# Optimization experiments

Hardware: AMD Instinct MI355X
Metric: run time of the kernel (lower is better)

Reference implementation:

```python
import jax, jax.numpy as jnp
import numpy as np

N = 100000
E = 3200000
IN_DIM = 64
HID = 64
G = 4096
BN_EPS = 1e-5


def setup_inputs() -> dict:
    key = jax.random.key(0)
    ks = jax.random.split(key, 20)
    def lin(k, fi, fo):
        bound = 1.0 / np.sqrt(fi)
        kw, kb = jax.random.split(k)
        W = jax.random.uniform(kw, (fi, fo), jnp.float32, -bound, bound)
        b = jax.random.uniform(kb, (fo,), jnp.float32, -bound, bound)
        return W, b
    x = jax.random.normal(ks[0], (N, IN_DIM), jnp.float32)
    edge_index = jax.random.randint(ks[1], (2, E), 0, N, jnp.int64)
    batch = jnp.sort(jax.random.randint(ks[2], (N,), 0, G, jnp.int64))
    proj_W, proj_b = lin(ks[3], IN_DIM, HID)
    conv1_W, conv1_b = lin(ks[4], HID, HID)
    conv2_W, conv2_b = lin(ks[5], HID, HID)
    conv3_W, conv3_b = lin(ks[6], HID, HID)
    head_W1, head_b1 = lin(ks[7], HID, HID // 2)
    head_W2, head_b2 = lin(ks[8], HID // 2, 1)
    ones = jnp.ones((HID,), jnp.float32)
    zeros = jnp.zeros((HID,), jnp.float32)
    return dict(
        x=x, edge_index=edge_index, batch=batch,
        proj_W=proj_W, proj_b=proj_b,
        conv1_W=conv1_W, conv1_b=conv1_b,
        conv2_W=conv2_W, conv2_b=conv2_b,
        conv3_W=conv3_W, conv3_b=conv3_b,
        bn1_g=ones, bn1_b=zeros, bn2_g=ones, bn2_b=zeros,
        bn3_g=ones, bn3_b=zeros,
        head_W1=head_W1, head_b1=head_b1,
        head_W2=head_W2, head_b2=head_b2,
    )


def _gcn_conv(x, W, b, src, dst, dinv):
    # GCNConv with self-loops and symmetric normalization (PyG semantics).
    xl = x @ W                                   # [N, H]
    norm = dinv[src] * dinv[dst]                 # [E]
    msg = xl[src] * norm[:, None]                # [E, H]  (memory-bound gather)
    agg = jax.ops.segment_sum(msg, dst, num_segments=x.shape[0])
    agg = agg + (dinv * dinv)[:, None] * xl      # self-loop contribution
    return agg + b


def _bn(h, g, b):
    mu = jnp.mean(h, axis=0)
    var = jnp.var(h, axis=0)
    return (h - mu) * jax.lax.rsqrt(var + BN_EPS) * g + b


def reference(x, edge_index, batch,
              proj_W, proj_b,
              conv1_W, conv1_b, conv2_W, conv2_b, conv3_W, conv3_b,
              bn1_g, bn1_b, bn2_g, bn2_b, bn3_g, bn3_b,
              head_W1, head_b1, head_W2, head_b2):
    src, dst = edge_index[0], edge_index[1]
    n = x.shape[0]
    # degree including self loop
    deg = jax.ops.segment_sum(jnp.ones_like(dst, jnp.float32), dst, num_segments=n) + 1.0
    dinv = jax.lax.rsqrt(deg)

    x0 = jax.nn.relu(x @ proj_W + proj_b)
    h = jax.nn.relu(_bn(_gcn_conv(x0, conv1_W, conv1_b, src, dst, dinv), bn1_g, bn1_b))
    h = jax.nn.relu(_bn(_gcn_conv(h, conv2_W, conv2_b, src, dst, dinv), bn2_g, bn2_b))
    h = h + x0
    h = jax.nn.relu(_bn(_gcn_conv(h, conv3_W, conv3_b, src, dst, dinv), bn3_g, bn3_b))

    # global mean pool over graphs
    sums = jax.ops.segment_sum(h, batch, num_segments=G)
    cnts = jax.ops.segment_sum(jnp.ones((n,), jnp.float32), batch, num_segments=G)
    pooled = sums / jnp.maximum(cnts, 1.0)[:, None]

    out = jax.nn.relu(pooled @ head_W1 + head_b1) @ head_W2 + head_b2
    return out.squeeze(-1)
```

## Files before the change

kernel.cpp:

```cpp
#include <hip/hip_runtime.h>
#include <hip/hip_fp16.h>

#define NNODES 100000
#define NEDGES 3200000
#define NGRAPH 4096
#define SBCNT 196
#define SBCAP 17504
#define P1CHUNK 4096
#define P1CAP 56
#define P1GRID 782
#define AGG_GRID 2048
#define BN_EPS 1e-5f
#define INV_N (1.0f / 100000.0f)

__global__ void k_zero_i(int* __restrict__ p, int n) {
  int i = blockIdx.x * blockDim.x + threadIdx.x;
  int st = gridDim.x * blockDim.x;
  for (; i < n; i += st) p[i] = 0;
}
__global__ void k_zero_f(float* __restrict__ p, int n) {
  int i = blockIdx.x * blockDim.x + threadIdx.x;
  int st = gridDim.x * blockDim.x;
  for (; i < n; i += st) p[i] = 0.0f;
}

__global__ void k_part1(const int* __restrict__ src, const int* __restrict__ dst,
                        int* __restrict__ sbcur, int* __restrict__ sbbuf, int e) {
  __shared__ int cnt[SBCNT];
  __shared__ int base[SBCNT];
  __shared__ int bins[SBCNT * P1CAP];
  int t = threadIdx.x;
  int start = blockIdx.x * P1CHUNK;
  int end = min(start + P1CHUNK, e);
  for (int i = t; i < SBCNT; i += 256) cnt[i] = 0;
  __syncthreads();
  for (int i = start + t; i < end; i += 256) {
    int s = src[i], d = dst[i];
    int sb = d >> 9;
    int en = (s << 9) | (d & 511);
    int pos = atomicAdd(&cnt[sb], 1);
    if (pos < P1CAP) {
      bins[sb * P1CAP + pos] = en;
    } else {
      int gp = atomicAdd(&sbcur[sb], 1);
      if (gp < SBCAP) sbbuf[(size_t)sb * SBCAP + gp] = en;
    }
  }
  __syncthreads();
  if (t < SBCNT) {
    int c = min(cnt[t], P1CAP);
    base[t] = (c > 0) ? atomicAdd(&sbcur[t], c) : 0;
  }
  __syncthreads();
  int lane = t & 63, wid = t >> 6;
  for (int b = wid; b < SBCNT; b += 4) {
    int c = min(cnt[b], P1CAP);
    if (lane < c) {
      int gp = base[b] + lane;
      if (gp < SBCAP) sbbuf[(size_t)b * SBCAP + gp] = bins[b * P1CAP + lane];
    }
  }
}

__global__ void k_part2(const int* __restrict__ sbcur, const int* __restrict__ sbbuf,
                        int* __restrict__ slots, int* __restrict__ deg,
                        int* __restrict__ rowstart, float* __restrict__ dinv) {
  __shared__ int cnt[512];
  __shared__ int pfx[512];
  __shared__ int cur[512];
  int sb = blockIdx.x;
  int t = threadIdx.x;
  int n = min(sbcur[sb], SBCAP);
  const int* __restrict__ pb = sbbuf + (size_t)sb * SBCAP;
  cnt[t] = 0;
  __syncthreads();
  for (int i = t; i < n; i += 512) atomicAdd(&cnt[pb[i] & 511], 1);
  __syncthreads();
  int myc = cnt[t];
  pfx[t] = myc;
  __syncthreads();
  for (int o = 1; o < 512; o <<= 1) {
    int x = (t >= o) ? pfx[t - o] : 0;
    __syncthreads();
    pfx[t] += x;
    __syncthreads();
  }
  int excl = pfx[t] - myc;
  int node = sb * 512 + t;
  if (node < NNODES) {
    deg[node] = myc;
    rowstart[node] = sb * SBCAP + excl;
    dinv[node] = rsqrtf((float)myc + 1.0f);
  }
  cur[t] = 0;
  __syncthreads();
  pfx[t] = excl;
  __syncthreads();
  for (int i = t; i < n; i += 512) {
    int e = pb[i];
    int dl = e & 511;
    int pos = atomicAdd(&cur[dl], 1);
    slots[(size_t)sb * SBCAP + pfx[dl] + pos] = e >> 9;
  }
}

template <int PRO, bool A_HALF, bool EPI_DINV, bool EPI_BR>
__global__ void k_gemm64(const void* __restrict__ Ain, const float* __restrict__ W,
                         const float* __restrict__ bias, const float* __restrict__ stats,
                         const float* __restrict__ g, const float* __restrict__ bb,
                         const __half* __restrict__ res, const float* __restrict__ dinv,
                         __half* __restrict__ C, int n) {
  __shared__ float Ws[64 * 64];
  __shared__ float As[64 * 64];
  __shared__ float scs[64], shs[64], bs[64];
  int t = threadIdx.x;
  {
    const float4* W4 = (const float4*)W;
    float4* Ws4 = (float4*)Ws;
    for (int i = t; i < 1024; i += 256) Ws4[i] = W4[i];
  }
  if (t < 64) {
    if (EPI_BR) bs[t] = bias[t];
    if (PRO >= 1) {
      float mu = stats[t] * INV_N;
      float var = stats[64 + t] * INV_N - mu * mu;
      float sc = g[t] * rsqrtf(var + BN_EPS);
      scs[t] = sc;
      shs[t] = bb[t] - mu * sc;
    }
  }
  int row0 = blockIdx.x * 64;
  int rows = min(64, n - row0);
  __syncthreads();
  if constexpr (A_HALF) {
    const __half2* A2 = (const __half2*)((const __half*)Ain + (size_t)row0 * 64);
    const __half2* R2 = (PRO == 2) ? (const __half2*)(res + (size_t)row0 * 64) : nullptr;
    for (int i = t; i < rows * 32; i += 256) {
      float2 f = __half22float2(A2[i]);
      int r = i >> 5;
      int c0 = (i & 31) * 2;
      if (PRO >= 1) {
        f.x = fmaxf(fmaf(f.x, scs[c0], shs[c0]), 0.0f);
        f.y = fmaxf(fmaf(f.y, scs[c0 + 1], shs[c0 + 1]), 0.0f);
        if (PRO == 2) {
          float2 r2 = __half22float2(R2[i]);
          f.x += r2.x;
          f.y += r2.y;
        }
      }
      As[r * 64 + c0] = f.x;
      As[r * 64 + c0 + 1] = f.y;
    }
  } else {
    const float4* A4 = (const float4*)((const float*)Ain + (size_t)row0 * 64);
    float4* As4 = (float4*)As;
    for (int i = t; i < rows * 16; i += 256) As4[i] = A4[i];
  }
  __syncthreads();
  int c = t & 63;
  int w = t >> 6;
  float acc[16];
#pragma unroll
  for (int j = 0; j < 16; ++j) acc[j] = 0.0f;
#pragma unroll 4
  for (int k = 0; k < 64; ++k) {
    float wv = Ws[(k << 6) + c];
#pragma unroll
    for (int j = 0; j < 16; ++j) {
      acc[j] = fmaf(As[((w + 4 * j) << 6) + k], wv, acc[j]);
    }
  }
#pragma unroll
  for (int j = 0; j < 16; ++j) {
    int r = w + 4 * j;
    if (r < rows) {
      float o = acc[j];
      if (EPI_BR) o = fmaxf(o + bs[c], 0.0f);
      if (EPI_DINV) o *= dinv[row0 + r];
      C[(size_t)(row0 + r) * 64 + c] = __float2half(o);
    }
  }
}

__global__ __launch_bounds__(256, 8)
void k_agg(const int* __restrict__ deg, const int* __restrict__ rowstart,
           const int* __restrict__ slots, const __half* __restrict__ y,
           const float* __restrict__ dinv, __half* __restrict__ ag,
           float* __restrict__ pstats) {
  int t = threadIdx.x;
  int lane = t & 63, wid = t >> 6;
  int wave = blockIdx.x * 4 + wid;
  int nw = gridDim.x * 4;
  float s = 0.0f, q = 0.0f;
  for (int node0 = wave; node0 < NNODES; node0 += nw) {
    int node = __builtin_amdgcn_readfirstlane(node0);
    int m = deg[node];
    const int* __restrict__ sp = slots + rowstart[node];
    float a0 = __half2float(y[(size_t)node * 64 + lane]);
    float a1 = 0.0f, a2 = 0.0f, a3 = 0.0f;
    float a4 = 0.0f, a5 = 0.0f, a6 = 0.0f, a7 = 0.0f;
    int k = 0;
    for (; k + 24 <= m; k += 24) {
      int i00 = sp[k + 0],  i01 = sp[k + 1],  i02 = sp[k + 2],  i03 = sp[k + 3];
      int i04 = sp[k + 4],  i05 = sp[k + 5],  i06 = sp[k + 6],  i07 = sp[k + 7];
      int i08 = sp[k + 8],  i09 = sp[k + 9],  i10 = sp[k + 10], i11 = sp[k + 11];
      int i12 = sp[k + 12], i13 = sp[k + 13], i14 = sp[k + 14], i15 = sp[k + 15];
      int i16 = sp[k + 16], i17 = sp[k + 17], i18 = sp[k + 18], i19 = sp[k + 19];
      int i20 = sp[k + 20], i21 = sp[k + 21], i22 = sp[k + 22], i23 = sp[k + 23];
      __half v00 = y[(size_t)i00 * 64 + lane];
      __half v01 = y[(size_t)i01 * 64 + lane];
      __half v02 = y[(size_t)i02 * 64 + lane];
      __half v03 = y[(size_t)i03 * 64 + lane];
      __half v04 = y[(size_t)i04 * 64 + lane];
      __half v05 = y[(size_t)i05 * 64 + lane];
      __half v06 = y[(size_t)i06 * 64 + lane];
      __half v07 = y[(size_t)i07 * 64 + lane];
      __half v08 = y[(size_t)i08 * 64 + lane];
      __half v09 = y[(size_t)i09 * 64 + lane];
      __half v10 = y[(size_t)i10 * 64 + lane];
      __half v11 = y[(size_t)i11 * 64 + lane];
      __half v12 = y[(size_t)i12 * 64 + lane];
      __half v13 = y[(size_t)i13 * 64 + lane];
      __half v14 = y[(size_t)i14 * 64 + lane];
      __half v15 = y[(size_t)i15 * 64 + lane];
      __half v16 = y[(size_t)i16 * 64 + lane];
      __half v17 = y[(size_t)i17 * 64 + lane];
      __half v18 = y[(size_t)i18 * 64 + lane];
      __half v19 = y[(size_t)i19 * 64 + lane];
      __half v20 = y[(size_t)i20 * 64 + lane];
      __half v21 = y[(size_t)i21 * 64 + lane];
      __half v22 = y[(size_t)i22 * 64 + lane];
      __half v23 = y[(size_t)i23 * 64 + lane];
      a0 += __half2float(v00); a1 += __half2float(v01);
      a2 += __half2float(v02); a3 += __half2float(v03);
      a4 += __half2float(v04); a5 += __half2float(v05);
      a6 += __half2float(v06); a7 += __half2float(v07);
      a0 += __half2float(v08); a1 += __half2float(v09);
      a2 += __half2float(v10); a3 += __half2float(v11);
      a4 += __half2float(v12); a5 += __half2float(v13);
      a6 += __half2float(v14); a7 += __half2float(v15);
      a0 += __half2float(v16); a1 += __half2float(v17);
      a2 += __half2float(v18); a3 += __half2float(v19);
      a4 += __half2float(v20); a5 += __half2float(v21);
      a6 += __half2float(v22); a7 += __half2float(v23);
    }
    for (; k + 8 <= m; k += 8) {
      int i0 = sp[k + 0], i1 = sp[k + 1], i2 = sp[k + 2], i3 = sp[k + 3];
      int i4 = sp[k + 4], i5 = sp[k + 5], i6 = sp[k + 6], i7 = sp[k + 7];
      __half v0 = y[(size_t)i0 * 64 + lane];
      __half v1 = y[(size_t)i1 * 64 + lane];
      __half v2 = y[(size_t)i2 * 64 + lane];
      __half v3 = y[(size_t)i3 * 64 + lane];
      __half v4 = y[(size_t)i4 * 64 + lane];
      __half v5 = y[(size_t)i5 * 64 + lane];
      __half v6 = y[(size_t)i6 * 64 + lane];
      __half v7 = y[(size_t)i7 * 64 + lane];
      a0 += __half2float(v0); a1 += __half2float(v1);
      a2 += __half2float(v2); a3 += __half2float(v3);
      a4 += __half2float(v4); a5 += __half2float(v5);
      a6 += __half2float(v6); a7 += __half2float(v7);
    }
    for (; k + 4 <= m; k += 4) {
      int i0 = sp[k + 0], i1 = sp[k + 1], i2 = sp[k + 2], i3 = sp[k + 3];
      __half v0 = y[(size_t)i0 * 64 + lane];
      __half v1 = y[(size_t)i1 * 64 + lane];
      __half v2 = y[(size_t)i2 * 64 + lane];
      __half v3 = y[(size_t)i3 * 64 + lane];
      a0 += __half2float(v0); a1 += __half2float(v1);
      a2 += __half2float(v2); a3 += __half2float(v3);
    }
    for (; k < m; ++k) a0 += __half2float(y[(size_t)sp[k] * 64 + lane]);
    float o = dinv[node] * (((a0 + a1) + (a2 + a3)) + ((a4 + a5) + (a6 + a7)));
    ag[(size_t)node0 * 64 + lane] = __float2half(o);
    s += o;
    q = fmaf(o, o, q);
  }
  __shared__ float ls[256], lq[256];
  ls[t] = s;
  lq[t] = q;
  __syncthreads();
  if (t < 64) {
    pstats[blockIdx.x * 128 + t] = ls[t] + ls[64 + t] + ls[128 + t] + ls[192 + t];
    pstats[blockIdx.x * 128 + 64 + t] = lq[t] + lq[64 + t] + lq[128 + t] + lq[192 + t];
  }
}

__global__ void k_stats_reduce(const float* __restrict__ pstats, float* __restrict__ stats) {
  __shared__ float red[256];
  int c = blockIdx.x;
  int t = threadIdx.x;
  float s = 0.0f;
  for (int i = t; i < AGG_GRID; i += 256) s += pstats[i * 128 + c];
  red[t] = s;
  __syncthreads();
  for (int o = 128; o >= 1; o >>= 1) {
    if (t < o) red[t] += red[t + o];
    __syncthreads();
  }
  if (t == 0) stats[c] = red[0];
}

__global__ void k_pool(const __half* __restrict__ ag, const float* __restrict__ stats,
                       const float* __restrict__ g, const float* __restrict__ bb,
                       const int* __restrict__ batch, float* __restrict__ psum,
                       float* __restrict__ pcnt) {
  int t = threadIdx.x, lane = t & 63;
  int wave = blockIdx.x * 4 + (t >> 6);
  int c0 = wave * 32;
  if (c0 >= NNODES) return;
  float mu = stats[lane] * INV_N;
  float var = stats[64 + lane] * INV_N - mu * mu;
  float sc = g[lane] * rsqrtf(var + BN_EPS);
  float sh = bb[lane] - mu * sc;
  int gprev = -1;
  float av = 0.0f, cv = 0.0f;
  int end = min(c0 + 32, NNODES);
  for (int node = c0; node < end; ++node) {
    int gi = batch[node];
    if (gi != gprev) {
      if (gprev >= 0) {
        atomicAdd(&psum[gprev * 64 + lane], av);
        if (lane == 0) atomicAdd(&pcnt[gprev], cv);
      }
      gprev = gi;
      av = 0.0f;
      cv = 0.0f;
    }
    av += fmaxf(fmaf(__half2float(ag[(size_t)node * 64 + lane]), sc, sh), 0.0f);
    cv += 1.0f;
  }
  if (gprev >= 0) {
    atomicAdd(&psum[gprev * 64 + lane], av);
    if (lane == 0) atomicAdd(&pcnt[gprev], cv);
  }
}

__global__ void k_head(const float* __restrict__ psum, const float* __restrict__ pcnt,
                       const float* __restrict__ W1, const float* __restrict__ b1,
                       const float* __restrict__ W2, const float* __restrict__ b2,
                       float* __restrict__ out) {
  int gidx = blockIdx.x;
  int t = threadIdx.x;
  __shared__ float pooled[64];
  __shared__ float hid[32];
  float cnt = fmaxf(pcnt[gidx], 1.0f);
  pooled[t] = psum[gidx * 64 + t] / cnt;
  __syncthreads();
  if (t < 32) {
    float a = b1[t];
#pragma unroll
    for (int k = 0; k < 64; ++k) a = fmaf(pooled[k], W1[k * 32 + t], a);
    hid[t] = fmaxf(a, 0.0f);
  }
  __syncthreads();
  if (t == 0) {
    float o = b2[0];
#pragma unroll
    for (int j = 0; j < 32; ++j) o = fmaf(hid[j], W2[j], o);
    out[gidx] = o;
  }
}

extern "C" void kernel_launch(void* const* d_in, const int* in_sizes, int n_in,
                              void* d_out, int out_size, void* d_ws, size_t ws_size,
                              hipStream_t stream) {
  const float* x       = (const float*)d_in[0];
  const int*   eidx    = (const int*)d_in[1];
  const int*   batch   = (const int*)d_in[2];
  const float* proj_W  = (const float*)d_in[3];
  const float* proj_b  = (const float*)d_in[4];
  const float* conv1_W = (const float*)d_in[5];
  const float* conv2_W = (const float*)d_in[7];
  const float* conv3_W = (const float*)d_in[9];
  const float* bn1_g   = (const float*)d_in[11];
  const float* bn1_b   = (const float*)d_in[12];
  const float* bn2_g   = (const float*)d_in[13];
  const float* bn2_b   = (const float*)d_in[14];
  const float* bn3_g   = (const float*)d_in[15];
  const float* bn3_b   = (const float*)d_in[16];
  const float* head_W1 = (const float*)d_in[17];
  const float* head_b1 = (const float*)d_in[18];
  const float* head_W2 = (const float*)d_in[19];
  const float* head_b2 = (const float*)d_in[20];
  float* out = (float*)d_out;

  const int N = NNODES, E = NEDGES, G = NGRAPH;
  const int* src = eidx;
  const int* dst = eidx + E;

  char* p = (char*)d_ws;
  auto align256 = [](size_t v) { return (v + 255) & ~(size_t)255; };
  int* sbcur = (int*)p;       p += align256((size_t)SBCNT * 4);
  int* deg = (int*)p;         p += align256((size_t)N * 4);
  int* rowstart = (int*)p;    p += align256((size_t)N * 4);
  int* slots = (int*)p;       p += align256((size_t)SBCNT * SBCAP * 4);
  float* dinv = (float*)p;    p += align256((size_t)N * 4);
  __half* x016 = (__half*)p;  p += align256((size_t)N * 64 * 2);
  __half* y16 = (__half*)p;   p += align256((size_t)N * 64 * 2);
  __half* ag16 = (__half*)p;  p += align256((size_t)N * 64 * 2);
  float* pstats = (float*)p;  p += align256((size_t)AGG_GRID * 128 * 4);
  float* stats1 = (float*)p;  p += align256(128 * 4);
  float* stats2 = (float*)p;  p += align256(128 * 4);
  float* stats3 = (float*)p;  p += align256(128 * 4);
  float* psum = (float*)p;    p += align256((size_t)G * 64 * 4);
  float* pcnt = (float*)p;    p += align256((size_t)G * 4);
  int* sbbuf = (int*)y16;

  const int TB = 256;
  int gemm_grid = (N + 63) / 64;

  k_zero_i<<<1, SBCNT, 0, stream>>>(sbcur, SBCNT);
  k_part1<<<P1GRID, TB, 0, stream>>>(src, dst, sbcur, sbbuf, E);
  k_part2<<<SBCNT, 512, 0, stream>>>(sbcur, sbbuf, slots, deg, rowstart, dinv);

  k_zero_f<<<(G * 64 + G + TB - 1) / TB, TB, 0, stream>>>(psum, G * 64 + G);

  k_gemm64<0, false, false, true><<<gemm_grid, TB, 0, stream>>>(
      x, proj_W, proj_b, nullptr, nullptr, nullptr, nullptr, nullptr, x016, N);

  k_gemm64<0, true, true, false><<<gemm_grid, TB, 0, stream>>>(
      x016, conv1_W, nullptr, nullptr, nullptr, nullptr, nullptr, dinv, y16, N);
  k_agg<<<AGG_GRID, TB, 0, stream>>>(deg, rowstart, slots, y16, dinv, ag16, pstats);
  k_stats_reduce<<<128, TB, 0, stream>>>(pstats, stats1);

  k_gemm64<1, true, true, false><<<gemm_grid, TB, 0, stream>>>(
      ag16, conv2_W, nullptr, stats1, bn1_g, bn1_b, nullptr, dinv, y16, N);
  k_agg<<<AGG_GRID, TB, 0, stream>>>(deg, rowstart, slots, y16, dinv, ag16, pstats);
  k_stats_reduce<<<128, TB, 0, stream>>>(pstats, stats2);

  k_gemm64<2, true, true, false><<<gemm_grid, TB, 0, stream>>>(
      ag16, conv3_W, nullptr, stats2, bn2_g, bn2_b, x016, dinv, y16, N);
  k_agg<<<AGG_GRID, TB, 0, stream>>>(deg, rowstart, slots, y16, dinv, ag16, pstats);
  k_stats_reduce<<<128, TB, 0, stream>>>(pstats, stats3);

  k_pool<<<(N + 127) / 128, TB, 0, stream>>>(ag16, stats3, bn3_g, bn3_b, batch, psum, pcnt);
  k_head<<<G, 64, 0, stream>>>(psum, pcnt, head_W1, head_b1, head_W2, head_b2, out);
}
```

Before: 396.5 us.

## Fuse BN stats reduction into aggregation via last-block ticket and merge zero kernels

Removes the three separate stats-reduce launches by having the last finishing aggregation block (found with an atomic ticket counter) sum the per-block partial statistics. Merges the two zeroing kernels into one that also clears the ticket counters, and prefetches the next node's degree, rowstart and dinv in the aggregation loop. This trades launch overhead for a serial tail reduction done by a single block of 128 threads plus extra fences.

```diff
diff --git a/kernel.cpp b/kernel.cpp
--- a/kernel.cpp
+++ b/kernel.cpp
@@ -13,15 +13,11 @@
 #define BN_EPS 1e-5f
 #define INV_N (1.0f / 100000.0f)
 
-__global__ void k_zero_i(int* __restrict__ p, int n) {
+__global__ void k_zero2(int* __restrict__ a, int na, int* __restrict__ b, int nb) {
   int i = blockIdx.x * blockDim.x + threadIdx.x;
   int st = gridDim.x * blockDim.x;
-  for (; i < n; i += st) p[i] = 0;
-}
-__global__ void k_zero_f(float* __restrict__ p, int n) {
-  int i = blockIdx.x * blockDim.x + threadIdx.x;
-  int st = gridDim.x * blockDim.x;
-  for (; i < n; i += st) p[i] = 0.0f;
+  for (int j = i; j < na; j += st) a[j] = 0;
+  for (int j = i; j < nb; j += st) b[j] = 0;
 }
 
 __global__ void k_part1(const int* __restrict__ src, const int* __restrict__ dst,
@@ -186,17 +182,35 @@
 void k_agg(const int* __restrict__ deg, const int* __restrict__ rowstart,
            const int* __restrict__ slots, const __half* __restrict__ y,
            const float* __restrict__ dinv, __half* __restrict__ ag,
-           float* __restrict__ pstats) {
+           float* __restrict__ pstats, float* __restrict__ stats,
+           int* __restrict__ ticket) {
   int t = threadIdx.x;
   int lane = t & 63, wid = t >> 6;
   int wave = blockIdx.x * 4 + wid;
   int nw = gridDim.x * 4;
   float s = 0.0f, q = 0.0f;
-  for (int node0 = wave; node0 < NNODES; node0 += nw) {
-    int node = __builtin_amdgcn_readfirstlane(node0);
-    int m = deg[node];
-    const int* __restrict__ sp = slots + rowstart[node];
-    float a0 = __half2float(y[(size_t)node * 64 + lane]);
+  int node0 = wave;
+  int pm = 0, prs = 0;
+  float pdv = 0.0f;
+  if (node0 < NNODES) {
+    int nn = __builtin_amdgcn_readfirstlane(node0);
+    pm = deg[nn];
+    prs = rowstart[nn];
+    pdv = dinv[nn];
+  }
+  for (; node0 < NNODES; node0 += nw) {
+    int m = pm;
+    int rs = prs;
+    float dv = pdv;
+    int nxt = node0 + nw;
+    if (nxt < NNODES) {
+      int nn = __builtin_amdgcn_readfirstlane(nxt);
+      pm = deg[nn];
+      prs = rowstart[nn];
+      pdv = dinv[nn];
+    }
+    const int* __restrict__ sp = slots + rs;
+    float a0 = __half2float(y[(size_t)node0 * 64 + lane]);
     float a1 = 0.0f, a2 = 0.0f, a3 = 0.0f;
     float a4 = 0.0f, a5 = 0.0f, a6 = 0.0f, a7 = 0.0f;
     int k = 0;
@@ -270,12 +284,13 @@
       a2 += __half2float(v2); a3 += __half2float(v3);
     }
     for (; k < m; ++k) a0 += __half2float(y[(size_t)sp[k] * 64 + lane]);
-    float o = dinv[node] * (((a0 + a1) + (a2 + a3)) + ((a4 + a5) + (a6 + a7)));
+    float o = dv * (((a0 + a1) + (a2 + a3)) + ((a4 + a5) + (a6 + a7)));
     ag[(size_t)node0 * 64 + lane] = __float2half(o);
     s += o;
     q = fmaf(o, o, q);
   }
   __shared__ float ls[256], lq[256];
+  __shared__ int isLast;
   ls[t] = s;
   lq[t] = q;
   __syncthreads();
@@ -283,21 +298,27 @@
     pstats[blockIdx.x * 128 + t] = ls[t] + ls[64 + t] + ls[128 + t] + ls[192 + t];
     pstats[blockIdx.x * 128 + 64 + t] = lq[t] + lq[64 + t] + lq[128 + t] + lq[192 + t];
   }
-}
-
-__global__ void k_stats_reduce(const float* __restrict__ pstats, float* __restrict__ stats) {
-  __shared__ float red[256];
-  int c = blockIdx.x;
-  int t = threadIdx.x;
-  float s = 0.0f;
-  for (int i = t; i < AGG_GRID; i += 256) s += pstats[i * 128 + c];
-  red[t] = s;
-  __syncthreads();
-  for (int o = 128; o >= 1; o >>= 1) {
-    if (t < o) red[t] += red[t + o];
-    __syncthreads();
-  }
-  if (t == 0) stats[c] = red[0];
+  __threadfence();
+  __syncthreads();
+  if (t == 0) isLast = (atomicAdd(ticket, 1) == (int)gridDim.x - 1) ? 1 : 0;
+  __syncthreads();
+  if (isLast) {
+    __threadfence();
+    if (t < 128) {
+      float S0 = 0, S1 = 0, S2 = 0, S3 = 0, S4 = 0, S5 = 0, S6 = 0, S7 = 0;
+      for (int i = 0; i < AGG_GRID; i += 8) {
+        S0 += pstats[(size_t)(i + 0) * 128 + t];
+        S1 += pstats[(size_t)(i + 1) * 128 + t];
+        S2 += pstats[(size_t)(i + 2) * 128 + t];
+        S3 += pstats[(size_t)(i + 3) * 128 + t];
+        S4 += pstats[(size_t)(i + 4) * 128 + t];
+        S5 += pstats[(size_t)(i + 5) * 128 + t];
+        S6 += pstats[(size_t)(i + 6) * 128 + t];
+        S7 += pstats[(size_t)(i + 7) * 128 + t];
+      }
+      stats[t] = ((S0 + S1) + (S2 + S3)) + ((S4 + S5) + (S6 + S7));
+    }
+  }
 }
 
 __global__ void k_pool(const __half* __restrict__ ag, const float* __restrict__ stats,
@@ -404,34 +425,36 @@
   float* stats3 = (float*)p;  p += align256(128 * 4);
   float* psum = (float*)p;    p += align256((size_t)G * 64 * 4);
   float* pcnt = (float*)p;    p += align256((size_t)G * 4);
+  int* tick = (int*)p;        p += align256(64 * 4);
   int* sbbuf = (int*)y16;
 
   const int TB = 256;
   int gemm_grid = (N + 63) / 64;
 
-  k_zero_i<<<1, SBCNT, 0, stream>>>(sbcur, SBCNT);
+  int zn2 = G * 64 + G + ((int)((char*)tick - (char*)pcnt) - G * 4) / 4 + 64;
+  k_zero2<<<(G * 64 + G + 64 + TB - 1) / TB, TB, 0, stream>>>(
+      sbcur, SBCNT, (int*)psum, zn2);
+
   k_part1<<<P1GRID, TB, 0, stream>>>(src, dst, sbcur, sbbuf, E);
   k_part2<<<SBCNT, 512, 0, stream>>>(sbcur, sbbuf, slots, deg, rowstart, dinv);
 
-  k_zero_f<<<(G * 64 + G + TB - 1) / TB, TB, 0, stream>>>(psum, G * 64 + G);
-
   k_gemm64<0, false, false, true><<<gemm_grid, TB, 0, stream>>>(
       x, proj_W, proj_b, nullptr, nullptr, nullptr, nullptr, nullptr, x016, N);
 
   k_gemm64<0, true, true, false><<<gemm_grid, TB, 0, stream>>>(
       x016, conv1_W, nullptr, nullptr, nullptr, nullptr, nullptr, dinv, y16, N);
-  k_agg<<<AGG_GRID, TB, 0, stream>>>(deg, rowstart, slots, y16, dinv, ag16, pstats);
-  k_stats_reduce<<<128, TB, 0, stream>>>(pstats, stats1);
+  k_agg<<<AGG_GRID, TB, 0, stream>>>(deg, rowstart, slots, y16, dinv, ag16,
+                                     pstats, stats1, tick + 0);
 
   k_gemm64<1, true, true, false><<<gemm_grid, TB, 0, stream>>>(
       ag16, conv2_W, nullptr, stats1, bn1_g, bn1_b, nullptr, dinv, y16, N);
-  k_agg<<<AGG_GRID, TB, 0, stream>>>(deg, rowstart, slots, y16, dinv, ag16, pstats);
-  k_stats_reduce<<<128, TB, 0, stream>>>(pstats, stats2);
+  k_agg<<<AGG_GRID, TB, 0, stream>>>(deg, rowstart, slots, y16, dinv, ag16,
+                                     pstats, stats2, tick + 1);
 
   k_gemm64<2, true, true, false><<<gemm_grid, TB, 0, stream>>>(
       ag16, conv3_W, nullptr, stats2, bn2_g, bn2_b, x016, dinv, y16, N);
-  k_agg<<<AGG_GRID, TB, 0, stream>>>(deg, rowstart, slots, y16, dinv, ag16, pstats);
-  k_stats_reduce<<<128, TB, 0, stream>>>(pstats, stats3);
+  k_agg<<<AGG_GRID, TB, 0, stream>>>(deg, rowstart, slots, y16, dinv, ag16,
+                                     pstats, stats3, tick + 2);
 
   k_pool<<<(N + 127) / 128, TB, 0, stream>>>(ag16, stats3, bn3_g, bn3_b, batch, psum, pcnt);
   k_head<<<G, 64, 0, stream>>>(psum, pcnt, head_W1, head_b1, head_W2, head_b2, out);
```

New measurement: 1.012 ms. 2.55x slower.
